# Optimization experiments

Measured on AMD Instinct MI355X. Metric: run time of the kernel, lower is better.

The kernel has to match this reference:

```python
import jax, jax.numpy as jnp
import numpy as np

N, E = 50000, 800000
IN_C, HID_C, OUT_C = 64, 64, 32
K, T = 2, 2  # num_stacks, num_layers (shared_weights=True)


def setup_inputs() -> dict:
    key = jax.random.key(0)
    ks = jax.random.split(key, 11)
    p = lambda k, shape, fan: jax.random.normal(k, shape, jnp.float32) / np.sqrt(fan)
    return {
        "x": jax.random.normal(ks[0], (N, IN_C), jnp.float32),
        "edge_index": jax.random.randint(ks[1], (2, E), 0, N, jnp.int32),
        # ARMAConv 1: in_c -> hid_c
        "init_w1": p(ks[2], (K, IN_C, HID_C), IN_C),
        "w1": p(ks[3], (1, K, HID_C, HID_C), HID_C),
        "root_w1": p(ks[4], (1, K, IN_C, HID_C), IN_C),
        "b1": 0.01 * jax.random.normal(ks[5], (1, K, 1, HID_C), jnp.float32),
        # ARMAConv 2: hid_c -> out_c
        "init_w2": p(ks[6], (K, HID_C, OUT_C), HID_C),
        "w2": p(ks[7], (1, K, OUT_C, OUT_C), OUT_C),
        "root_w2": p(ks[8], (1, K, HID_C, OUT_C), HID_C),
        "b2": 0.01 * jax.random.normal(ks[9], (1, K, 1, OUT_C), jnp.float32),
    }


def _gcn_norm(src, dst, num_nodes):
    # PyG gcn_norm with add_self_loops=False, edge_weight = 1
    deg = jax.ops.segment_sum(jnp.ones(src.shape[0], jnp.float32), dst,
                              num_segments=num_nodes)
    dinv = jnp.where(deg > 0, deg ** -0.5, 0.0)
    return dinv[src] * dinv[dst]  # [E]


def _arma_conv(x, src, dst, norm, init_w, w, root_w, b, num_nodes):
    # x: [N, F_in]; shared weights across layers, act=ReLU, eval mode (no dropout)
    root = jnp.einsum('nf,kfg->nkg', x, root_w[0]) + b[0, :, 0, :]  # [N,K,Fout]
    out = x
    for t in range(T):
        if t == 0:
            out = jnp.einsum('nf,kfg->nkg', out, init_w)        # [N,K,Fout]
        else:
            out = jnp.einsum('nkf,kfg->nkg', out, w[0])          # [N,K,Fout]
        msg = out[src] * norm[:, None, None]                      # [E,K,Fout]
        out = jax.ops.segment_sum(msg, dst, num_segments=num_nodes)
        out = jax.nn.relu(out + root)
    return out.mean(axis=1)  # mean over stacks -> [N, Fout]


def reference(x, edge_index, init_w1, w1, root_w1, b1, init_w2, w2, root_w2, b2):
    src, dst = edge_index[0], edge_index[1]
    norm = _gcn_norm(src, dst, N)
    h = jax.nn.relu(_arma_conv(x, src, dst, norm, init_w1, w1, root_w1, b1, N))
    # F.dropout is identity in eval mode
    return _arma_conv(h, src, dst, norm, init_w2, w2, root_w2, b2, N)
```

## Files before the change

### kernel.cpp

```cpp
#include <hip/hip_runtime.h>
#include <cstdint>
#include <cstddef>


#define NN 50000
#define EE 800000
#define NCHUNK ((NN + 255) / 256)

__device__ __forceinline__ float rl(float v, int l) {
  return __int_as_float(__builtin_amdgcn_readlane(__float_as_int(v), l));
}

__device__ __forceinline__ float bcast(const float4& a, int c) {
  int sl = c >> 2;
  switch (c & 3) {
    case 0: return rl(a.x, sl);
    case 1: return rl(a.y, sl);
    case 2: return rl(a.z, sl);
    default: return rl(a.w, sl);
  }
}

__device__ __forceinline__ void red4(float4& a) {
#pragma unroll
  for (int off = 16; off < 64; off <<= 1) {
    a.x += __shfl_xor(a.x, off);
    a.y += __shfl_xor(a.y, off);
    a.z += __shfl_xor(a.z, off);
    a.w += __shfl_xor(a.w, off);
  }
}

__device__ __forceinline__ void acc4(float4& a, const float4& v) {
  a.x += v.x; a.y += v.y; a.z += v.z; a.w += v.w;
}


__global__ __launch_bounds__(256) void k_degree(const int* __restrict__ dst,
                                                int* __restrict__ deg) {
  int i = blockIdx.x * 256 + threadIdx.x;
  if (i < EE) atomicAdd(&deg[dst[i]], 1);
}

__global__ __launch_bounds__(256) void k_part(const int* __restrict__ deg,
                                              int* __restrict__ partial) {
  int i = blockIdx.x * 256 + threadIdx.x;
  int v = (i < NN) ? deg[i] : 0;
#pragma unroll
  for (int off = 1; off < 64; off <<= 1) v += __shfl_xor(v, off);
  __shared__ int wsum[4];
  if ((threadIdx.x & 63) == 0) wsum[threadIdx.x >> 6] = v;
  __syncthreads();
  if (threadIdx.x == 0) partial[blockIdx.x] = wsum[0] + wsum[1] + wsum[2] + wsum[3];
}

__global__ __launch_bounds__(256) void k_scanp(const int* __restrict__ partial,
                                               int* __restrict__ chunkbase) {
  __shared__ int sc[256];
  int t = threadIdx.x;
  int v = (t < NCHUNK) ? partial[t] : 0;
  sc[t] = v;
  __syncthreads();
  for (int off = 1; off < 256; off <<= 1) {
    int u = (t >= off) ? sc[t - off] : 0;
    __syncthreads();
    sc[t] += u;
    __syncthreads();
  }
  if (t < NCHUNK) chunkbase[t] = sc[t] - v;
}

__global__ __launch_bounds__(256) void k_rows(const int* __restrict__ deg,
                                              const int* __restrict__ chunkbase,
                                              int* __restrict__ rowstart,
                                              float* __restrict__ dinv,
                                              int* __restrict__ cursor) {
  __shared__ int sc[256];
  int t = threadIdx.x;
  int i = blockIdx.x * 256 + t;
  int d = (i < NN) ? deg[i] : 0;
  sc[t] = d;
  __syncthreads();
  for (int off = 1; off < 256; off <<= 1) {
    int u = (t >= off) ? sc[t - off] : 0;
    __syncthreads();
    sc[t] += u;
    __syncthreads();
  }
  if (i < NN) {
    rowstart[i] = chunkbase[blockIdx.x] + sc[t] - d;
    dinv[i] = (d > 0) ? rsqrtf((float)d) : 0.f;
    cursor[i] = 0;
  }
  if (blockIdx.x == 0 && t == 0) rowstart[NN] = EE;
}

__global__ __launch_bounds__(256) void k_fill(const int* __restrict__ src,
                                              const int* __restrict__ dst,
                                              const int* __restrict__ rowstart,
                                              int* __restrict__ cursor,
                                              int* __restrict__ csr) {
  int i = blockIdx.x * 256 + threadIdx.x;
  if (i < EE) {
    int d = dst[i];
    int pos = rowstart[d] + atomicAdd(&cursor[d], 1);
    csr[pos] = src[i];
  }
}


__global__ __launch_bounds__(256) void k_aggx(const float* __restrict__ x,
                                              const float* __restrict__ dinv,
                                              const int* __restrict__ rowstart,
                                              const int* __restrict__ csr,
                                              float* __restrict__ outp) {
  int lane = threadIdx.x & 63;
  int f4 = lane & 15, es = lane >> 4;
  int wid = (blockIdx.x * 256 + threadIdx.x) >> 6;
  int nw = (gridDim.x * 256) >> 6;
  const float4* x4 = (const float4*)x;
  for (int n = wid; n < NN; n += nw) {
    int beg = rowstart[n], end = rowstart[n + 1];
    float4 a = {0.f, 0.f, 0.f, 0.f}, b = {0.f, 0.f, 0.f, 0.f};
    int j = beg + es;
    for (; j + 4 < end; j += 8) {
      int s0 = csr[j], s1 = csr[j + 4];
      float d0 = dinv[s0], d1 = dinv[s1];
      float4 v0 = x4[(size_t)s0 * 16 + f4];
      float4 v1 = x4[(size_t)s1 * 16 + f4];
      a.x = fmaf(v0.x, d0, a.x); a.y = fmaf(v0.y, d0, a.y);
      a.z = fmaf(v0.z, d0, a.z); a.w = fmaf(v0.w, d0, a.w);
      b.x = fmaf(v1.x, d1, b.x); b.y = fmaf(v1.y, d1, b.y);
      b.z = fmaf(v1.z, d1, b.z); b.w = fmaf(v1.w, d1, b.w);
    }
    if (j < end) {
      int s = csr[j];
      float d = dinv[s];
      float4 v = x4[(size_t)s * 16 + f4];
      a.x = fmaf(v.x, d, a.x); a.y = fmaf(v.y, d, a.y);
      a.z = fmaf(v.z, d, a.z); a.w = fmaf(v.w, d, a.w);
    }
    acc4(a, b);
    red4(a);
    if (lane < 16) {
      float dn = dinv[n];
      a.x *= dn; a.y *= dn; a.z *= dn; a.w *= dn;
      ((float4*)outp)[(size_t)n * 16 + f4] = a;
    }
  }
}


__global__ __launch_bounds__(256) void k_t0(const float* __restrict__ x,
                                            const float* __restrict__ aggxs,
                                            const float* __restrict__ initW,
                                            const float* __restrict__ rootW,
                                            const float* __restrict__ bias,
                                            const float* __restrict__ dinv,
                                            float* __restrict__ root01,
                                            float* __restrict__ s01) {
  __shared__ float Wi[8192];
  __shared__ float Wr[8192];
  for (int i = threadIdx.x; i < 8192; i += 256) { Wi[i] = initW[i]; Wr[i] = rootW[i]; }
  __syncthreads();
  int lane = threadIdx.x & 63;
  float b_0 = bias[lane], b_1 = bias[64 + lane];
  int wid = (blockIdx.x * 256 + threadIdx.x) >> 6;
  int nw = (gridDim.x * 256) >> 6;
  for (int n = wid; n < NN; n += nw) {
    float dn = dinv[n];
    float xv = x[(size_t)n * 64 + lane];
    float gv = aggxs[(size_t)n * 64 + lane];
    float r0 = b_0, r1 = b_1;
    float i0 = 0.f, i1 = 0.f;
#pragma unroll
    for (int c = 0; c < 64; c++) {
      float xc = rl(xv, c), gc = rl(gv, c);
      r0 = fmaf(xc, Wr[c * 64 + lane], r0);
      r1 = fmaf(xc, Wr[4096 + c * 64 + lane], r1);
      i0 = fmaf(gc, Wi[c * 64 + lane], i0);
      i1 = fmaf(gc, Wi[4096 + c * 64 + lane], i1);
    }
    size_t b = (size_t)n * 128 + lane;
    root01[b] = r0;
    root01[b + 64] = r1;
    s01[b] = fmaxf(i0 + r0, 0.f) * dn;
    s01[b + 64] = fmaxf(i1 + r1, 0.f) * dn;
  }
}


__global__ __launch_bounds__(256) void k_t1(const float* __restrict__ s01,
                                            const float* __restrict__ root01,
                                            const float* __restrict__ W,
                                            const float* __restrict__ dinv,
                                            const int* __restrict__ rowstart,
                                            const int* __restrict__ csr,
                                            float* __restrict__ h,
                                            float* __restrict__ hs) {
  __shared__ float Ws[8192];
  for (int i = threadIdx.x; i < 8192; i += 256) Ws[i] = W[i];
  __syncthreads();
  int lane = threadIdx.x & 63;
  int f4 = lane & 15, es = lane >> 4;
  int wid = (blockIdx.x * 256 + threadIdx.x) >> 6;
  int nw = (gridDim.x * 256) >> 6;
  const float4* in4 = (const float4*)s01;
  for (int n = wid; n < NN; n += nw) {
    int beg = rowstart[n], end = rowstart[n + 1];
    float4 a0 = {0.f, 0.f, 0.f, 0.f}, a1 = {0.f, 0.f, 0.f, 0.f};
    int j = beg + es;
    for (; j + 4 < end; j += 8) {
      int s0 = csr[j], s1 = csr[j + 4];
      const float4* r0 = in4 + (size_t)s0 * 32;
      const float4* r1 = in4 + (size_t)s1 * 32;
      float4 v00 = r0[f4], v01 = r0[16 + f4];
      float4 v10 = r1[f4], v11 = r1[16 + f4];
      acc4(a0, v00); acc4(a1, v01);
      acc4(a0, v10); acc4(a1, v11);
    }
    if (j < end) {
      int s = csr[j];
      const float4* r = in4 + (size_t)s * 32;
      float4 v0 = r[f4], v1 = r[16 + f4];
      acc4(a0, v0); acc4(a1, v1);
    }
    red4(a0);
    red4(a1);
    float dn = dinv[n];
    float c0 = 0.f, c1 = 0.f;
#pragma unroll
    for (int c = 0; c < 64; c++) {
      c0 = fmaf(bcast(a0, c), Ws[c * 64 + lane], c0);
      c1 = fmaf(bcast(a1, c), Ws[4096 + c * 64 + lane], c1);
    }
    size_t b = (size_t)n * 128 + lane;
    float o0 = fmaxf(fmaf(dn, c0, root01[b]), 0.f);
    float o1 = fmaxf(fmaf(dn, c1, root01[b + 64]), 0.f);
    float hv = 0.5f * (o0 + o1);
    h[(size_t)n * 64 + lane] = hv;
    hs[(size_t)n * 64 + lane] = hv * dn;
  }
}


__global__ __launch_bounds__(256) void k2_t0(const float* __restrict__ h,
                                             const float* __restrict__ hs,
                                             const float* __restrict__ initW2,
                                             const float* __restrict__ rootW2,
                                             const float* __restrict__ b2,
                                             const float* __restrict__ dinv,
                                             const int* __restrict__ rowstart,
                                             const int* __restrict__ csr,
                                             float* __restrict__ root2,
                                             float* __restrict__ s2) {
  __shared__ float Wi[4096];
  __shared__ float Wr[4096];
  for (int i = threadIdx.x; i < 4096; i += 256) { Wi[i] = initW2[i]; Wr[i] = rootW2[i]; }
  __syncthreads();
  int lane = threadIdx.x & 63;
  int f4 = lane & 15, es = lane >> 4;
  int k = lane >> 5, col = lane & 31;
  float bv = b2[lane];
  int wid = (blockIdx.x * 256 + threadIdx.x) >> 6;
  int nw = (gridDim.x * 256) >> 6;
  const float4* in4 = (const float4*)hs;
  for (int n = wid; n < NN; n += nw) {
    int beg = rowstart[n], end = rowstart[n + 1];
    float4 a = {0.f, 0.f, 0.f, 0.f}, b = {0.f, 0.f, 0.f, 0.f};
    int j = beg + es;
    for (; j + 4 < end; j += 8) {
      int s0 = csr[j], s1 = csr[j + 4];
      float4 v0 = in4[(size_t)s0 * 16 + f4];
      float4 v1 = in4[(size_t)s1 * 16 + f4];
      acc4(a, v0); acc4(b, v1);
    }
    if (j < end) {
      int s = csr[j];
      acc4(a, in4[(size_t)s * 16 + f4]);
    }
    acc4(a, b);
    red4(a);
    float dn = dinv[n];
    float hv = h[(size_t)n * 64 + lane];
    float accR = bv;
    float accI = 0.f;
#pragma unroll
    for (int c = 0; c < 64; c++) {
      float xc = rl(hv, c);
      float gc = bcast(a, c);
      accR = fmaf(xc, Wr[k * 2048 + c * 32 + col], accR);
      accI = fmaf(gc, Wi[k * 2048 + c * 32 + col], accI);
    }
    float o = fmaxf(fmaf(dn, accI, accR), 0.f);
    root2[(size_t)n * 64 + lane] = accR;
    s2[(size_t)n * 64 + lane] = o * dn;
  }
}


__global__ __launch_bounds__(256) void k2_t1(const float* __restrict__ s2,
                                             const float* __restrict__ root2,
                                             const float* __restrict__ W2,
                                             const float* __restrict__ dinv,
                                             const int* __restrict__ rowstart,
                                             const int* __restrict__ csr,
                                             float* __restrict__ outp) {
  __shared__ float Ws[2048];
  for (int i = threadIdx.x; i < 2048; i += 256) Ws[i] = W2[i];
  __syncthreads();
  int lane = threadIdx.x & 63;
  int f4 = lane & 15, es = lane >> 4;
  int k = lane >> 5, col = lane & 31;
  int wid = (blockIdx.x * 256 + threadIdx.x) >> 6;
  int nw = (gridDim.x * 256) >> 6;
  const float4* in4 = (const float4*)s2;
  for (int n = wid; n < NN; n += nw) {
    int beg = rowstart[n], end = rowstart[n + 1];
    float4 a = {0.f, 0.f, 0.f, 0.f}, b = {0.f, 0.f, 0.f, 0.f};
    int j = beg + es;
    for (; j + 4 < end; j += 8) {
      int s0 = csr[j], s1 = csr[j + 4];
      float4 v0 = in4[(size_t)s0 * 16 + f4];
      float4 v1 = in4[(size_t)s1 * 16 + f4];
      acc4(a, v0); acc4(b, v1);
    }
    if (j < end) {
      int s = csr[j];
      acc4(a, in4[(size_t)s * 16 + f4]);
    }
    acc4(a, b);
    red4(a);
    float dn = dinv[n];
    float acc = 0.f;
#pragma unroll
    for (int c = 0; c < 32; c++) {
      float p0 = bcast(a, c);
      float p1 = bcast(a, 32 + c);
      float pc = (lane < 32) ? p0 : p1;
      acc = fmaf(pc, Ws[k * 1024 + c * 32 + col], acc);
    }
    float o = fmaxf(fmaf(dn, acc, root2[(size_t)n * 64 + lane]), 0.f);
    o += __shfl_xor(o, 32);
    if (lane < 32) outp[(size_t)n * 32 + col] = 0.5f * o;
  }
}


extern "C" void kernel_launch(void* const* d_in, const int* in_sizes, int n_in,
                              void* d_out, int out_size, void* d_ws, size_t ws_size,
                              hipStream_t stream) {
  const float* x = (const float*)d_in[0];
  const int* edge_index = (const int*)d_in[1];
  const float* initW1 = (const float*)d_in[2];
  const float* w1 = (const float*)d_in[3];
  const float* rootW1 = (const float*)d_in[4];
  const float* b1 = (const float*)d_in[5];
  const float* initW2 = (const float*)d_in[6];
  const float* w2 = (const float*)d_in[7];
  const float* rootW2 = (const float*)d_in[8];
  const float* b2 = (const float*)d_in[9];
  float* out = (float*)d_out;

  const int* src = edge_index;
  const int* dst = edge_index + EE;

  size_t off = 0;
  auto carve = [&](size_t bytes) {
    size_t r = off;
    off = (off + bytes + 255) & ~(size_t)255;
    return r;
  };
  char* ws = (char*)d_ws;
  int* deg = (int*)(ws + carve((size_t)NN * 4));
  int* rowstart = (int*)(ws + carve((size_t)(NN + 1) * 4));
  int* csr = (int*)(ws + carve((size_t)EE * 4));
  float* dinv = (float*)(ws + carve((size_t)NN * 4));
  int* cursor = (int*)(ws + carve((size_t)NN * 4));
  int* partial = (int*)(ws + carve(256 * 4));
  int* chunkbase = (int*)(ws + carve(256 * 4));
  float* B1 = (float*)(ws + carve((size_t)NN * 64 * 4));
  float* B2 = (float*)(ws + carve((size_t)NN * 128 * 4));
  float* B3 = (float*)(ws + carve((size_t)NN * 128 * 4));
  float* B4 = (float*)(ws + carve((size_t)NN * 64 * 4));
  (void)ws_size; (void)in_sizes; (void)n_in; (void)out_size;

  const int EB = (EE + 255) / 256;

  hipMemsetAsync(deg, 0, (size_t)NN * 4, stream);
  k_degree<<<EB, 256, 0, stream>>>(dst, deg);
  k_part<<<NCHUNK, 256, 0, stream>>>(deg, partial);
  k_scanp<<<1, 256, 0, stream>>>(partial, chunkbase);
  k_rows<<<NCHUNK, 256, 0, stream>>>(deg, chunkbase, rowstart, dinv, cursor);
  k_fill<<<EB, 256, 0, stream>>>(src, dst, rowstart, cursor, csr);

  k_aggx<<<1536, 256, 0, stream>>>(x, dinv, rowstart, csr, B1);
  k_t0<<<1024, 256, 0, stream>>>(x, B1, initW1, rootW1, b1, dinv, B2, B3);
  k_t1<<<1280, 256, 0, stream>>>(B3, B2, w1, dinv, rowstart, csr, B1, B4);
  k2_t0<<<1280, 256, 0, stream>>>(B1, B4, initW2, rootW2, b2, dinv, rowstart, csr, B2, B3);
  k2_t1<<<1536, 256, 0, stream>>>(B3, B2, w2, dinv, rowstart, csr, out);
}
```

Baseline: 469.4 us.

## Process four nodes per wavefront in gather kernels, amortizing weight loads across nodes

```diff
diff --git a/kernel.cpp b/kernel.cpp
--- a/kernel.cpp
+++ b/kernel.cpp
@@ -5,34 +5,21 @@
 
 #define NN 50000
 #define EE 800000
+#define NG (NN / 4)
 #define NCHUNK ((NN + 255) / 256)
 
 __device__ __forceinline__ float rl(float v, int l) {
   return __int_as_float(__builtin_amdgcn_readlane(__float_as_int(v), l));
 }
 
-__device__ __forceinline__ float bcast(const float4& a, int c) {
-  int sl = c >> 2;
+__device__ __forceinline__ float slotb(const float4& a, int i, int c) {
+  int sl = i * 16 + (c >> 2);
   switch (c & 3) {
     case 0: return rl(a.x, sl);
     case 1: return rl(a.y, sl);
     case 2: return rl(a.z, sl);
     default: return rl(a.w, sl);
   }
-}
-
-__device__ __forceinline__ void red4(float4& a) {
-#pragma unroll
-  for (int off = 16; off < 64; off <<= 1) {
-    a.x += __shfl_xor(a.x, off);
-    a.y += __shfl_xor(a.y, off);
-    a.z += __shfl_xor(a.z, off);
-    a.w += __shfl_xor(a.w, off);
-  }
-}
-
-__device__ __forceinline__ void acc4(float4& a, const float4& v) {
-  a.x += v.x; a.y += v.y; a.z += v.z; a.w += v.w;
 }
 
 
@@ -108,6 +95,15 @@
   }
 }
 
+#define GATHER_SETUP(base)                                  \
+  int n = (base) + es;                                      \
+  int j = rowstart[n];                                      \
+  int end = rowstart[n + 1];                                \
+  int dg = end - j;                                         \
+  int mtmp = max(dg, __shfl_xor(dg, 16));                   \
+  mtmp = max(mtmp, __shfl_xor(mtmp, 32));                   \
+  int mx = __builtin_amdgcn_readfirstlane(mtmp);
+
 
 __global__ __launch_bounds__(256) void k_aggx(const float* __restrict__ x,
                                               const float* __restrict__ dinv,
@@ -116,37 +112,29 @@
                                               float* __restrict__ outp) {
   int lane = threadIdx.x & 63;
   int f4 = lane & 15, es = lane >> 4;
-  int wid = (blockIdx.x * 256 + threadIdx.x) >> 6;
-  int nw = (gridDim.x * 256) >> 6;
+  int wg = (blockIdx.x * 256 + threadIdx.x) >> 6;
+  int nwv = (gridDim.x * 256) >> 6;
   const float4* x4 = (const float4*)x;
-  for (int n = wid; n < NN; n += nw) {
-    int beg = rowstart[n], end = rowstart[n + 1];
-    float4 a = {0.f, 0.f, 0.f, 0.f}, b = {0.f, 0.f, 0.f, 0.f};
-    int j = beg + es;
-    for (; j + 4 < end; j += 8) {
-      int s0 = csr[j], s1 = csr[j + 4];
-      float d0 = dinv[s0], d1 = dinv[s1];
+  for (int g = wg; g < NG; g += nwv) {
+    int base = g * 4;
+    GATHER_SETUP(base);
+    float4 a = {0.f, 0.f, 0.f, 0.f};
+    for (int it = 0; it < mx; it += 2) {
+      int jj0 = min(j, EE - 1), jj1 = min(j + 1, EE - 1);
+      int s0 = csr[jj0], s1 = csr[jj1];
+      float w0 = (j < end) ? dinv[s0] : 0.f;
+      float w1 = (j + 1 < end) ? dinv[s1] : 0.f;
       float4 v0 = x4[(size_t)s0 * 16 + f4];
       float4 v1 = x4[(size_t)s1 * 16 + f4];
-      a.x = fmaf(v0.x, d0, a.x); a.y = fmaf(v0.y, d0, a.y);
-      a.z = fmaf(v0.z, d0, a.z); a.w = fmaf(v0.w, d0, a.w);
-      b.x = fmaf(v1.x, d1, b.x); b.y = fmaf(v1.y, d1, b.y);
-      b.z = fmaf(v1.z, d1, b.z); b.w = fmaf(v1.w, d1, b.w);
-    }
-    if (j < end) {
-      int s = csr[j];
-      float d = dinv[s];
-      float4 v = x4[(size_t)s * 16 + f4];
-      a.x = fmaf(v.x, d, a.x); a.y = fmaf(v.y, d, a.y);
-      a.z = fmaf(v.z, d, a.z); a.w = fmaf(v.w, d, a.w);
-    }
-    acc4(a, b);
-    red4(a);
-    if (lane < 16) {
-      float dn = dinv[n];
-      a.x *= dn; a.y *= dn; a.z *= dn; a.w *= dn;
-      ((float4*)outp)[(size_t)n * 16 + f4] = a;
-    }
+      a.x = fmaf(v0.x, w0, a.x); a.y = fmaf(v0.y, w0, a.y);
+      a.z = fmaf(v0.z, w0, a.z); a.w = fmaf(v0.w, w0, a.w);
+      a.x = fmaf(v1.x, w1, a.x); a.y = fmaf(v1.y, w1, a.y);
+      a.z = fmaf(v1.z, w1, a.z); a.w = fmaf(v1.w, w1, a.w);
+      j += 2;
+    }
+    float dn = dinv[n];
+    a.x *= dn; a.y *= dn; a.z *= dn; a.w *= dn;
+    ((float4*)outp)[(size_t)n * 16 + f4] = a;
   }
 }
 
@@ -203,43 +191,54 @@
   __syncthreads();
   int lane = threadIdx.x & 63;
   int f4 = lane & 15, es = lane >> 4;
-  int wid = (blockIdx.x * 256 + threadIdx.x) >> 6;
-  int nw = (gridDim.x * 256) >> 6;
+  int wg = (blockIdx.x * 256 + threadIdx.x) >> 6;
+  int nwv = (gridDim.x * 256) >> 6;
   const float4* in4 = (const float4*)s01;
-  for (int n = wid; n < NN; n += nw) {
-    int beg = rowstart[n], end = rowstart[n + 1];
-    float4 a0 = {0.f, 0.f, 0.f, 0.f}, a1 = {0.f, 0.f, 0.f, 0.f};
-    int j = beg + es;
-    for (; j + 4 < end; j += 8) {
-      int s0 = csr[j], s1 = csr[j + 4];
+  for (int g = wg; g < NG; g += nwv) {
+    int base = g * 4;
+    GATHER_SETUP(base);
+    float4 a = {0.f, 0.f, 0.f, 0.f}, b = {0.f, 0.f, 0.f, 0.f};
+    for (int it = 0; it < mx; it += 2) {
+      int jj0 = min(j, EE - 1), jj1 = min(j + 1, EE - 1);
+      int s0 = csr[jj0], s1 = csr[jj1];
+      float m0 = (j < end) ? 1.f : 0.f;
+      float m1 = (j + 1 < end) ? 1.f : 0.f;
       const float4* r0 = in4 + (size_t)s0 * 32;
       const float4* r1 = in4 + (size_t)s1 * 32;
       float4 v00 = r0[f4], v01 = r0[16 + f4];
       float4 v10 = r1[f4], v11 = r1[16 + f4];
-      acc4(a0, v00); acc4(a1, v01);
-      acc4(a0, v10); acc4(a1, v11);
-    }
-    if (j < end) {
-      int s = csr[j];
-      const float4* r = in4 + (size_t)s * 32;
-      float4 v0 = r[f4], v1 = r[16 + f4];
-      acc4(a0, v0); acc4(a1, v1);
-    }
-    red4(a0);
-    red4(a1);
-    float dn = dinv[n];
-    float c0 = 0.f, c1 = 0.f;
+      a.x = fmaf(v00.x, m0, a.x); a.y = fmaf(v00.y, m0, a.y);
+      a.z = fmaf(v00.z, m0, a.z); a.w = fmaf(v00.w, m0, a.w);
+      b.x = fmaf(v01.x, m0, b.x); b.y = fmaf(v01.y, m0, b.y);
+      b.z = fmaf(v01.z, m0, b.z); b.w = fmaf(v01.w, m0, b.w);
+      a.x = fmaf(v10.x, m1, a.x); a.y = fmaf(v10.y, m1, a.y);
+      a.z = fmaf(v10.z, m1, a.z); a.w = fmaf(v10.w, m1, a.w);
+      b.x = fmaf(v11.x, m1, b.x); b.y = fmaf(v11.y, m1, b.y);
+      b.z = fmaf(v11.z, m1, b.z); b.w = fmaf(v11.w, m1, b.w);
+      j += 2;
+    }
+    float c0[4] = {0.f, 0.f, 0.f, 0.f}, c1[4] = {0.f, 0.f, 0.f, 0.f};
 #pragma unroll
     for (int c = 0; c < 64; c++) {
-      c0 = fmaf(bcast(a0, c), Ws[c * 64 + lane], c0);
-      c1 = fmaf(bcast(a1, c), Ws[4096 + c * 64 + lane], c1);
-    }
-    size_t b = (size_t)n * 128 + lane;
-    float o0 = fmaxf(fmaf(dn, c0, root01[b]), 0.f);
-    float o1 = fmaxf(fmaf(dn, c1, root01[b + 64]), 0.f);
-    float hv = 0.5f * (o0 + o1);
-    h[(size_t)n * 64 + lane] = hv;
-    hs[(size_t)n * 64 + lane] = hv * dn;
+      float w0 = Ws[c * 64 + lane];
+      float w1 = Ws[4096 + c * 64 + lane];
+#pragma unroll
+      for (int i = 0; i < 4; i++) {
+        c0[i] = fmaf(slotb(a, i, c), w0, c0[i]);
+        c1[i] = fmaf(slotb(b, i, c), w1, c1[i]);
+      }
+    }
+    float dnl = dinv[n];
+#pragma unroll
+    for (int i = 0; i < 4; i++) {
+      float dni = rl(dnl, i * 16);
+      size_t bb = (size_t)(base + i) * 128 + lane;
+      float o0 = fmaxf(fmaf(dni, c0[i], root01[bb]), 0.f);
+      float o1 = fmaxf(fmaf(dni, c1[i], root01[bb + 64]), 0.f);
+      float hv = 0.5f * (o0 + o1);
+      h[(size_t)(base + i) * 64 + lane] = hv;
+      hs[(size_t)(base + i) * 64 + lane] = hv * dni;
+    }
   }
 }
 
@@ -262,39 +261,48 @@
   int f4 = lane & 15, es = lane >> 4;
   int k = lane >> 5, col = lane & 31;
   float bv = b2[lane];
-  int wid = (blockIdx.x * 256 + threadIdx.x) >> 6;
-  int nw = (gridDim.x * 256) >> 6;
+  int wg = (blockIdx.x * 256 + threadIdx.x) >> 6;
+  int nwv = (gridDim.x * 256) >> 6;
   const float4* in4 = (const float4*)hs;
-  for (int n = wid; n < NN; n += nw) {
-    int beg = rowstart[n], end = rowstart[n + 1];
-    float4 a = {0.f, 0.f, 0.f, 0.f}, b = {0.f, 0.f, 0.f, 0.f};
-    int j = beg + es;
-    for (; j + 4 < end; j += 8) {
-      int s0 = csr[j], s1 = csr[j + 4];
+  for (int g = wg; g < NG; g += nwv) {
+    int base = g * 4;
+    GATHER_SETUP(base);
+    float4 a = {0.f, 0.f, 0.f, 0.f};
+    for (int it = 0; it < mx; it += 2) {
+      int jj0 = min(j, EE - 1), jj1 = min(j + 1, EE - 1);
+      int s0 = csr[jj0], s1 = csr[jj1];
+      float m0 = (j < end) ? 1.f : 0.f;
+      float m1 = (j + 1 < end) ? 1.f : 0.f;
       float4 v0 = in4[(size_t)s0 * 16 + f4];
       float4 v1 = in4[(size_t)s1 * 16 + f4];
-      acc4(a, v0); acc4(b, v1);
-    }
-    if (j < end) {
-      int s = csr[j];
-      acc4(a, in4[(size_t)s * 16 + f4]);
-    }
-    acc4(a, b);
-    red4(a);
-    float dn = dinv[n];
-    float hv = h[(size_t)n * 64 + lane];
-    float accR = bv;
-    float accI = 0.f;
+      a.x = fmaf(v0.x, m0, a.x); a.y = fmaf(v0.y, m0, a.y);
+      a.z = fmaf(v0.z, m0, a.z); a.w = fmaf(v0.w, m0, a.w);
+      a.x = fmaf(v1.x, m1, a.x); a.y = fmaf(v1.y, m1, a.y);
+      a.z = fmaf(v1.z, m1, a.z); a.w = fmaf(v1.w, m1, a.w);
+      j += 2;
+    }
+    float hv[4];
+#pragma unroll
+    for (int i = 0; i < 4; i++) hv[i] = h[(size_t)(base + i) * 64 + lane];
+    float aR[4] = {bv, bv, bv, bv}, aI[4] = {0.f, 0.f, 0.f, 0.f};
 #pragma unroll
     for (int c = 0; c < 64; c++) {
-      float xc = rl(hv, c);
-      float gc = bcast(a, c);
-      accR = fmaf(xc, Wr[k * 2048 + c * 32 + col], accR);
-      accI = fmaf(gc, Wi[k * 2048 + c * 32 + col], accI);
-    }
-    float o = fmaxf(fmaf(dn, accI, accR), 0.f);
-    root2[(size_t)n * 64 + lane] = accR;
-    s2[(size_t)n * 64 + lane] = o * dn;
+      float wr = Wr[k * 2048 + c * 32 + col];
+      float wi = Wi[k * 2048 + c * 32 + col];
+#pragma unroll
+      for (int i = 0; i < 4; i++) {
+        aR[i] = fmaf(rl(hv[i], c), wr, aR[i]);
+        aI[i] = fmaf(slotb(a, i, c), wi, aI[i]);
+      }
+    }
+    float dnl = dinv[n];
+#pragma unroll
+    for (int i = 0; i < 4; i++) {
+      float dni = rl(dnl, i * 16);
+      float o = fmaxf(fmaf(dni, aI[i], aR[i]), 0.f);
+      root2[(size_t)(base + i) * 64 + lane] = aR[i];
+      s2[(size_t)(base + i) * 64 + lane] = o * dni;
+    }
   }
 }
 
@@ -312,37 +320,46 @@
   int lane = threadIdx.x & 63;
   int f4 = lane & 15, es = lane >> 4;
   int k = lane >> 5, col = lane & 31;
-  int wid = (blockIdx.x * 256 + threadIdx.x) >> 6;
-  int nw = (gridDim.x * 256) >> 6;
+  int wg = (blockIdx.x * 256 + threadIdx.x) >> 6;
+  int nwv = (gridDim.x * 256) >> 6;
   const float4* in4 = (const float4*)s2;
-  for (int n = wid; n < NN; n += nw) {
-    int beg = rowstart[n], end = rowstart[n + 1];
-    float4 a = {0.f, 0.f, 0.f, 0.f}, b = {0.f, 0.f, 0.f, 0.f};
-    int j = beg + es;
-    for (; j + 4 < end; j += 8) {
-      int s0 = csr[j], s1 = csr[j + 4];
+  for (int g = wg; g < NG; g += nwv) {
+    int base = g * 4;
+    GATHER_SETUP(base);
+    float4 a = {0.f, 0.f, 0.f, 0.f};
+    for (int it = 0; it < mx; it += 2) {
+      int jj0 = min(j, EE - 1), jj1 = min(j + 1, EE - 1);
+      int s0 = csr[jj0], s1 = csr[jj1];
+      float m0 = (j < end) ? 1.f : 0.f;
+      float m1 = (j + 1 < end) ? 1.f : 0.f;
       float4 v0 = in4[(size_t)s0 * 16 + f4];
       float4 v1 = in4[(size_t)s1 * 16 + f4];
-      acc4(a, v0); acc4(b, v1);
-    }
-    if (j < end) {
-      int s = csr[j];
-      acc4(a, in4[(size_t)s * 16 + f4]);
-    }
-    acc4(a, b);
-    red4(a);
-    float dn = dinv[n];
-    float acc = 0.f;
+      a.x = fmaf(v0.x, m0, a.x); a.y = fmaf(v0.y, m0, a.y);
+      a.z = fmaf(v0.z, m0, a.z); a.w = fmaf(v0.w, m0, a.w);
+      a.x = fmaf(v1.x, m1, a.x); a.y = fmaf(v1.y, m1, a.y);
+      a.z = fmaf(v1.z, m1, a.z); a.w = fmaf(v1.w, m1, a.w);
+      j += 2;
+    }
+    float acc[4] = {0.f, 0.f, 0.f, 0.f};
 #pragma unroll
     for (int c = 0; c < 32; c++) {
-      float p0 = bcast(a, c);
-      float p1 = bcast(a, 32 + c);
-      float pc = (lane < 32) ? p0 : p1;
-      acc = fmaf(pc, Ws[k * 1024 + c * 32 + col], acc);
-    }
-    float o = fmaxf(fmaf(dn, acc, root2[(size_t)n * 64 + lane]), 0.f);
-    o += __shfl_xor(o, 32);
-    if (lane < 32) outp[(size_t)n * 32 + col] = 0.5f * o;
+      float w = Ws[k * 1024 + c * 32 + col];
+#pragma unroll
+      for (int i = 0; i < 4; i++) {
+        float p0 = slotb(a, i, c);
+        float p1 = slotb(a, i, 32 + c);
+        float pc = (lane < 32) ? p0 : p1;
+        acc[i] = fmaf(pc, w, acc[i]);
+      }
+    }
+    float dnl = dinv[n];
+#pragma unroll
+    for (int i = 0; i < 4; i++) {
+      float dni = rl(dnl, i * 16);
+      float o = fmaxf(fmaf(dni, acc[i], root2[(size_t)(base + i) * 64 + lane]), 0.f);
+      o += __shfl_xor(o, 32);
+      if (lane < 32) outp[(size_t)(base + i) * 32 + col] = 0.5f * o;
+    }
   }
 }
 
@@ -394,7 +411,7 @@
   k_rows<<<NCHUNK, 256, 0, stream>>>(deg, chunkbase, rowstart, dinv, cursor);
   k_fill<<<EB, 256, 0, stream>>>(src, dst, rowstart, cursor, csr);
 
-  k_aggx<<<1536, 256, 0, stream>>>(x, dinv, rowstart, csr, B1);
+  k_aggx<<<3125, 256, 0, stream>>>(x, dinv, rowstart, csr, B1);
   k_t0<<<1024, 256, 0, stream>>>(x, B1, initW1, rootW1, b1, dinv, B2, B3);
   k_t1<<<1280, 256, 0, stream>>>(B3, B2, w1, dinv, rowstart, csr, B1, B4);
   k2_t0<<<1280, 256, 0, stream>>>(B1, B4, initW2, rootW2, b2, dinv, rowstart, csr, B2, B3);
```

New measurement: 481.1 us. +2.5%, slower.
